# Optimization experiments

Measured on AMD Instinct MI355X. Metric: run time of the kernel, lower is better.

The kernel has to match this reference:

```python
import jax, jax.numpy as jnp
import numpy as np

B, N, D = 4096, 20, 256
MAX_STEPS = int(N * 1.5)  # exploration_ratio = 1.5


def setup_inputs() -> dict:
    key = jax.random.key(0)
    ks = jax.random.split(key, 9)
    s = 1.0 / np.sqrt(D)
    u = lambda k, shape: jax.random.uniform(k, shape, jnp.float32, -s, s)
    return {
        "node_emb": jax.random.normal(ks[0], (B, N, D), jnp.float32),
        "mask": jnp.ones((B, N), jnp.bool_),  # present in signature, unused by forward
        "W_ih": u(ks[1], (4 * D, D)),
        "W_hh": u(ks[2], (4 * D, D)),
        "b_ih": u(ks[3], (4 * D,)),
        "b_hh": u(ks[4], (4 * D,)),
        "attn_w": u(ks[5], (D, D)),
        "attn_b": u(ks[6], (D,)),
        "done_w": u(ks[7], (D,)),
        "done_b": u(ks[8], ()),
        "revisit_penalty": jnp.float32(-0.05),
        "greedy": 1,
    }


def reference(node_emb, mask, W_ih, W_hh, b_ih, b_hh, attn_w, attn_b, done_w, done_b, revisit_penalty, greedy):
    Bx, Nx, Dx = node_emb.shape
    aB = jnp.arange(Bx)
    aN = jnp.arange(Nx)
    scale = 1.0 / jnp.sqrt(jnp.float32(Dx))
    keys = node_emb @ attn_w.T + attn_b  # [B, N, D], loop-invariant

    def step(carry, t):
        h, c, inp, visited, unique, complete, first = carry
        # LSTMCell (PyTorch gate order i, f, g, o)
        gates = inp @ W_ih.T + b_ih + h @ W_hh.T + b_hh
        i, f, g, o = jnp.split(gates, 4, axis=1)
        c2 = jax.nn.sigmoid(f) * c + jax.nn.sigmoid(i) * jnp.tanh(g)
        h2 = jax.nn.sigmoid(o) * jnp.tanh(c2)
        # done predictor (greedy: complete when sigmoid > 0.5)
        done_p = jax.nn.sigmoid(h2 @ done_w + done_b)  # [B]
        eligible = (~complete) & (unique >= Nx) & (t >= Nx)
        complete2 = complete | (eligible & (done_p > 0.5))
        # pointer scores
        scores = jnp.einsum('bd,bnd->bn', h2, keys) * scale
        rev = ((~complete2) & (unique < Nx))[:, None] & visited
        scores = jnp.where(rev, revisit_penalty, scores)
        scores = jnp.where(complete2[:, None], jnp.float32(-1e9), scores)
        scores = jnp.where(complete2[:, None] & (aN[None, :] == first[:, None]), jnp.float32(100.0), scores)
        probs = jax.nn.softmax(scores, axis=1)
        choice = jnp.argmax(probs, axis=1).astype(jnp.int32)
        curr = jnp.where(complete2, first, choice)
        logp = jnp.log(probs[aB, curr] + 1e-10)
        first2 = jnp.where(t == 0, curr, first)
        newly = (~complete2) & (~visited[aB, curr])
        unique2 = unique + newly.astype(jnp.int32)
        visited2 = visited.at[aB, curr].set(visited[aB, curr] | (~complete2))
        inp2 = node_emb[aB, curr]
        return (h2, c2, inp2, visited2, unique2, complete2, first2), (curr, logp)

    init = (
        jnp.zeros((Bx, Dx), jnp.float32),
        jnp.zeros((Bx, Dx), jnp.float32),
        node_emb.mean(axis=1),
        jnp.zeros((Bx, Nx), jnp.bool_),
        jnp.zeros((Bx,), jnp.int32),
        jnp.zeros((Bx,), jnp.bool_),
        jnp.zeros((Bx,), jnp.int32),
    )
    carry, (tours_t, logps_t) = jax.lax.scan(step, init, jnp.arange(MAX_STEPS))
    complete, first = carry[5], carry[6]
    # step == max_steps: incomplete tours are closed at first_node, log-prob 0
    final_node = jnp.where(~complete, first, jnp.int32(0))
    tours = jnp.concatenate([tours_t.T, final_node[:, None]], axis=1)   # [B, MAX_STEPS+1]
    logps = jnp.concatenate([logps_t.T, jnp.zeros((Bx, 1), jnp.float32)], axis=1)
    return tours, logps
```

## Files before the change

### kernel.cpp

```cpp
#include <hip/hip_runtime.h>
#include <cstdint>
#include <cstddef>

#define NB   4096
#define NN   20
#define DD   256
#define TST  30
#define RPB  16
#define NTHR 512
#define SCALE 0.0625f

__device__ __forceinline__ float sigf(float x) {
    return 1.0f / (1.0f + expf(-x));
}

__global__ __launch_bounds__(256) void keys_gemm(
    const float* __restrict__ A, const float* __restrict__ W,
    const float* __restrict__ bias, float* __restrict__ C)
{
    __shared__ float As[64][33];
    __shared__ float Bs[64][33];
    const int bm = blockIdx.x * 64;
    const int bn = blockIdx.y * 64;
    const int t  = threadIdx.x;
    const int tm = t >> 4, tn = t & 15;
    const int sr = t >> 3;
    const int sk = (t & 7) << 2;
    float acc[4][4] = {};
    for (int k0 = 0; k0 < DD; k0 += 32) {
        __syncthreads();
#pragma unroll
        for (int p = 0; p < 2; ++p) {
            const int r = sr + p * 32;
            const float4 va = *(const float4*)&A[(size_t)(bm + r) * DD + k0 + sk];
            As[r][sk] = va.x; As[r][sk + 1] = va.y; As[r][sk + 2] = va.z; As[r][sk + 3] = va.w;
            const float4 vb = *(const float4*)&W[(size_t)(bn + r) * DD + k0 + sk];
            Bs[r][sk] = vb.x; Bs[r][sk + 1] = vb.y; Bs[r][sk + 2] = vb.z; Bs[r][sk + 3] = vb.w;
        }
        __syncthreads();
#pragma unroll
        for (int k = 0; k < 32; ++k) {
            float a[4], b[4];
#pragma unroll
            for (int i = 0; i < 4; ++i) a[i] = As[tm * 4 + i][k];
#pragma unroll
            for (int j = 0; j < 4; ++j) b[j] = Bs[tn * 4 + j][k];
#pragma unroll
            for (int i = 0; i < 4; ++i)
#pragma unroll
                for (int j = 0; j < 4; ++j)
                    acc[i][j] = fmaf(a[i], b[j], acc[i][j]);
        }
    }
#pragma unroll
    for (int i = 0; i < 4; ++i) {
        const int row = bm + tm * 4 + i;
#pragma unroll
        for (int j = 0; j < 4; ++j) {
            const int col = bn + tn * 4 + j;
            C[(size_t)row * DD + col] = acc[i][j] + bias[col];
        }
    }
}

__global__ __launch_bounds__(512) void decode(
    const float* __restrict__ ne,
    const float* __restrict__ wih,
    const float* __restrict__ whh,
    const float* __restrict__ bih,
    const float* __restrict__ bhh,
    const float* __restrict__ dwv,
    const float* __restrict__ dbp,
    const float* __restrict__ rpp,
    const float* __restrict__ keys,
    float* __restrict__ out)
{
    __shared__ float xcat[RPB][512];
    __shared__ float cst[RPB][DD];
    __shared__ float wt[512 * 32];
    __shared__ unsigned vis[RPB];
    __shared__ int uniq[RPB];
    __shared__ int firstn[RPB];
    __shared__ int compl_[RPB];

    const int t    = threadIdx.x;
    const int b0   = blockIdx.x * RPB;
    const int mg   = t >> 7;
    const int ni3  = t & 127;
    const int w    = t >> 6;
    const int lane = t & 63;

    const float done_b = dbp[0];
    const float rp     = rpp[0];

    float bsv[8];
#pragma unroll
    for (int g = 0; g < 8; ++g) {
        const int j = (g >> 1) * 256 + ((g & 1) << 7) + ni3;
        bsv[g] = bih[j] + bhh[j];
    }

    for (int idx = t; idx < RPB * DD; idx += NTHR) {
        const int r = idx >> 8, d = idx & 255;
        xcat[r][256 + d] = 0.0f;
        cst[r][d] = 0.0f;
    }
#pragma unroll
    for (int rr = 0; rr < 2; ++rr) {
        const int r = w * 2 + rr;
        const int b = b0 + r;
        float sx = 0.f, sy = 0.f, sz = 0.f, sw = 0.f;
        for (int n = 0; n < NN; ++n) {
            const float4 v = *(const float4*)&ne[((size_t)b * NN + n) * DD + lane * 4];
            sx += v.x; sy += v.y; sz += v.z; sw += v.w;
        }
        float4 m4;
        m4.x = sx / 20.0f; m4.y = sy / 20.0f; m4.z = sz / 20.0f; m4.w = sw / 20.0f;
        *(float4*)&xcat[r][lane * 4] = m4;
    }
    if (t < RPB) { vis[t] = 0u; uniq[t] = 0; firstn[t] = 0; compl_[t] = 0; }
    __syncthreads();

    auto stage = [&](int half, int k0) {
        __syncthreads();
        const float* base = (k0 < 256) ? (wih + k0) : (whh + (k0 - 256));
        const int rl = t >> 3;
        const int q4 = t & 7;
#pragma unroll
        for (int p = 0; p < 8; ++p) {
            const int row = rl + (p << 6);
            const float4 v = *(const float4*)&base[(size_t)(half * 512 + row) * DD + (q4 << 2)];
            *(float4*)&wt[(row << 5) + ((q4 ^ (row & 7)) << 2)] = v;
        }
        __syncthreads();
    };

    auto gemm_chunk = [&](int k0, float (&acc)[4][4]) {
#pragma unroll
        for (int q = 0; q < 8; ++q) {
            float4 av[4];
#pragma unroll
            for (int i = 0; i < 4; ++i)
                av[i] = *(const float4*)&xcat[(mg << 2) + i][k0 + (q << 2)];
            float4 wv[4];
#pragma unroll
            for (int c = 0; c < 4; ++c) {
                const int row = ni3 + (c << 7);
                wv[c] = *(const float4*)&wt[(row << 5) + ((q ^ (row & 7)) << 2)];
            }
#pragma unroll
            for (int i = 0; i < 4; ++i)
#pragma unroll
                for (int c = 0; c < 4; ++c) {
                    acc[i][c] = fmaf(av[i].x, wv[c].x, acc[i][c]);
                    acc[i][c] = fmaf(av[i].y, wv[c].y, acc[i][c]);
                    acc[i][c] = fmaf(av[i].z, wv[c].z, acc[i][c]);
                    acc[i][c] = fmaf(av[i].w, wv[c].w, acc[i][c]);
                }
        }
    };

    for (int step = 0; step < TST; ++step) {
        float acc0[4][4] = {};
        float acc1[4][4] = {};
#pragma unroll 1
        for (int kc = 0; kc < 16; ++kc) { stage(0, kc * 32); gemm_chunk(kc * 32, acc0); }
#pragma unroll 1
        for (int kc = 0; kc < 16; ++kc) { stage(1, kc * 32); gemm_chunk(kc * 32, acc1); }
        __syncthreads();

#pragma unroll
        for (int i = 0; i < 4; ++i) {
            const int r = (mg << 2) + i;
#pragma unroll
            for (int dd = 0; dd < 2; ++dd) {
                const int d = ni3 + (dd << 7);
                const float gi = acc0[i][dd]     + bsv[0 + dd];
                const float gf = acc0[i][2 + dd] + bsv[2 + dd];
                const float gg = acc1[i][dd]     + bsv[4 + dd];
                const float go = acc1[i][2 + dd] + bsv[6 + dd];
                const float co = cst[r][d];
                const float cn = sigf(gf) * co + sigf(gi) * tanhf(gg);
                const float hn = sigf(go) * tanhf(cn);
                cst[r][d] = cn;
                xcat[r][256 + d] = hn;
            }
        }
        __syncthreads();

#pragma unroll
        for (int rr = 0; rr < 2; ++rr) {
            const int r = w * 2 + rr;
            const int b = b0 + r;
            const float4 h4 = *(const float4*)&xcat[r][256 + lane * 4];

            const float4 dv = *(const float4*)&dwv[lane * 4];
            float pd = h4.x * dv.x + h4.y * dv.y + h4.z * dv.z + h4.w * dv.w;
#pragma unroll
            for (int o = 32; o >= 1; o >>= 1) pd += __shfl_xor(pd, o);

            float myscore = 0.0f;
            for (int n = 0; n < NN; ++n) {
                const float4 kv = *(const float4*)&keys[((size_t)b * NN + n) * DD + lane * 4];
                float sc = h4.x * kv.x + h4.y * kv.y + h4.z * kv.z + h4.w * kv.w;
#pragma unroll
                for (int o = 32; o >= 1; o >>= 1) sc += __shfl_xor(sc, o);
                if (lane == n) myscore = sc;
            }

            const unsigned vm0 = vis[r];
            int un = uniq[r];
            int fn = firstn[r];
            const int cm = compl_[r];

            const float dprob = 1.0f / (1.0f + expf(-(pd + done_b)));
            const int eligible = (!cm) && (un >= NN) && (step >= NN);
            const int cm2 = cm || (eligible && (dprob > 0.5f));

            float s;
            if (lane < NN) {
                s = myscore * SCALE;
                if ((!cm2) && (un < NN) && ((vm0 >> lane) & 1u)) s = rp;
                if (cm2) s = (lane == fn) ? 100.0f : -1e9f;
            } else {
                s = -INFINITY;
            }
            float m = s;
#pragma unroll
            for (int o = 32; o >= 1; o >>= 1) m = fmaxf(m, __shfl_xor(m, o));
            const float e = (lane < NN) ? expf(s - m) : 0.0f;
            float se = e;
#pragma unroll
            for (int o = 32; o >= 1; o >>= 1) se += __shfl_xor(se, o);
            const float p = e / se;
            float pm = p;
#pragma unroll
            for (int o = 32; o >= 1; o >>= 1) pm = fmaxf(pm, __shfl_xor(pm, o));
            const unsigned long long bal = __ballot(p == pm);
            const int choice = __ffsll(bal) - 1;
            const int curr = cm2 ? fn : choice;
            const float pc = __shfl(p, curr);
            const float lp = logf(pc + 1e-10f);

            if (step == 0) fn = curr;
            const int newly = (!cm2) && !((vm0 >> curr) & 1u);
            unsigned vm = vm0;
            if (!cm2) vm |= (1u << curr);
            un += newly;

            if (lane == 0) {
                vis[r] = vm; uniq[r] = un; firstn[r] = fn; compl_[r] = cm2;
                out[(size_t)b * (TST + 1) + step] = (float)curr;
                out[(size_t)NB * (TST + 1) + (size_t)b * (TST + 1) + step] = lp;
            }
            const float4 nv = *(const float4*)&ne[((size_t)b * NN + curr) * DD + lane * 4];
            *(float4*)&xcat[r][lane * 4] = nv;
        }
    }

    __syncthreads();
    if (t < RPB) {
        const int b = b0 + t;
        out[(size_t)b * (TST + 1) + TST] = compl_[t] ? 0.0f : (float)firstn[t];
        out[(size_t)NB * (TST + 1) + (size_t)b * (TST + 1) + TST] = 0.0f;
    }
}

extern "C" void kernel_launch(void* const* d_in, const int* in_sizes, int n_in,
                              void* d_out, int out_size, void* d_ws, size_t ws_size,
                              hipStream_t stream) {
    (void)in_sizes; (void)n_in; (void)out_size;
    const float* ne  = (const float*)d_in[0];
    const float* wih = (const float*)d_in[2];
    const float* whh = (const float*)d_in[3];
    const float* bih = (const float*)d_in[4];
    const float* bhh = (const float*)d_in[5];
    const float* aw  = (const float*)d_in[6];
    const float* ab  = (const float*)d_in[7];
    const float* dw  = (const float*)d_in[8];
    const float* db  = (const float*)d_in[9];
    const float* rp  = (const float*)d_in[10];
    float* out  = (float*)d_out;
    float* keys = (float*)d_ws;
    if (ws_size < (size_t)NB * NN * DD * sizeof(float)) return;

    keys_gemm<<<dim3((NB * NN) / 64, DD / 64), 256, 0, stream>>>(ne, aw, ab, keys);
    decode<<<dim3(NB / RPB), NTHR, 0, stream>>>(ne, wih, whh, bih, bhh, dw, db, rp, keys, out);
}
```

Baseline: 5.221 ms.

## Stream LSTM weights from global into registers with split-K halves, drop LDS staging

Replaces the per-chunk LDS staging of W_ih/W_hh, which cost two block barriers per chunk, with direct register loads that are double-buffered. Each thread computes 16 rows by 4 gate columns over one K half (input or hidden), and the two halves are reduced through a shared gates buffer. Cell state and the per-row tour state move into registers. The pointer softmax is now computed per lane over all 20 nodes, removing the shuffle reductions. This raises register pressure to about 64 accumulators plus 16 float4 weights, and requests 2 blocks per CU via launch bounds, which may cause spills.

```diff
diff --git a/kernel.cpp b/kernel.cpp
--- a/kernel.cpp
+++ b/kernel.cpp
@@ -63,7 +63,7 @@
     }
 }
 
-__global__ __launch_bounds__(512) void decode(
+__global__ __launch_bounds__(NTHR, 2) void decode(
     const float* __restrict__ ne,
     const float* __restrict__ wih,
     const float* __restrict__ whh,
@@ -76,19 +76,17 @@
     float* __restrict__ out)
 {
     __shared__ float xcat[RPB][512];
-    __shared__ float cst[RPB][DD];
-    __shared__ float wt[512 * 32];
-    __shared__ unsigned vis[RPB];
-    __shared__ int uniq[RPB];
-    __shared__ int firstn[RPB];
-    __shared__ int compl_[RPB];
+    __shared__ float gates[RPB][1024];
 
     const int t    = threadIdx.x;
     const int b0   = blockIdx.x * RPB;
+    const int lane = t & 63;
+    const int w    = t >> 6;
+    const int kh   = t >> 8;
+    const int q    = (t >> 6) & 3;
     const int mg   = t >> 7;
     const int ni3  = t & 127;
-    const int w    = t >> 6;
-    const int lane = t & 63;
+    const int xb   = kh << 8;
 
     const float done_b = dbp[0];
     const float rp     = rpp[0];
@@ -99,12 +97,16 @@
         const int j = (g >> 1) * 256 + ((g & 1) << 7) + ni3;
         bsv[g] = bih[j] + bhh[j];
     }
-
-    for (int idx = t; idx < RPB * DD; idx += NTHR) {
-        const int r = idx >> 8, d = idx & 255;
-        xcat[r][256 + d] = 0.0f;
-        cst[r][d] = 0.0f;
-    }
+    const float4 dv = *(const float4*)&dwv[lane * 4];
+
+    const float* Wb = kh ? whh : wih;
+    const float* p0 = Wb + (size_t)(q * 256 + 0 * 64 + lane) * DD;
+    const float* p1 = Wb + (size_t)(q * 256 + 1 * 64 + lane) * DD;
+    const float* p2 = Wb + (size_t)(q * 256 + 2 * 64 + lane) * DD;
+    const float* p3 = Wb + (size_t)(q * 256 + 3 * 64 + lane) * DD;
+
+    for (int idx = t; idx < RPB * 256; idx += NTHR)
+        xcat[idx >> 8][256 + (idx & 255)] = 0.0f;
 #pragma unroll
     for (int rr = 0; rr < 2; ++rr) {
         const int r = w * 2 + rr;
@@ -118,55 +120,75 @@
         m4.x = sx / 20.0f; m4.y = sy / 20.0f; m4.z = sz / 20.0f; m4.w = sw / 20.0f;
         *(float4*)&xcat[r][lane * 4] = m4;
     }
-    if (t < RPB) { vis[t] = 0u; uniq[t] = 0; firstn[t] = 0; compl_[t] = 0; }
-    __syncthreads();
-
-    auto stage = [&](int half, int k0) {
-        __syncthreads();
-        const float* base = (k0 < 256) ? (wih + k0) : (whh + (k0 - 256));
-        const int rl = t >> 3;
-        const int q4 = t & 7;
-#pragma unroll
-        for (int p = 0; p < 8; ++p) {
-            const int row = rl + (p << 6);
-            const float4 v = *(const float4*)&base[(size_t)(half * 512 + row) * DD + (q4 << 2)];
-            *(float4*)&wt[(row << 5) + ((q4 ^ (row & 7)) << 2)] = v;
-        }
-        __syncthreads();
+
+    float creg[4][2] = {};
+    unsigned vm[2] = {0u, 0u};
+    int un[2] = {0, 0}, fn[2] = {0, 0}, cm[2] = {0, 0};
+
+    auto ldw = [&](int k, float4 (&W)[4][2]) {
+#pragma unroll
+        for (int j = 0; j < 2; ++j) {
+            W[0][j] = *(const float4*)(p0 + k + j * 4);
+            W[1][j] = *(const float4*)(p1 + k + j * 4);
+            W[2][j] = *(const float4*)(p2 + k + j * 4);
+            W[3][j] = *(const float4*)(p3 + k + j * 4);
+        }
     };
 
-    auto gemm_chunk = [&](int k0, float (&acc)[4][4]) {
-#pragma unroll
-        for (int q = 0; q < 8; ++q) {
-            float4 av[4];
-#pragma unroll
-            for (int i = 0; i < 4; ++i)
-                av[i] = *(const float4*)&xcat[(mg << 2) + i][k0 + (q << 2)];
-            float4 wv[4];
-#pragma unroll
-            for (int c = 0; c < 4; ++c) {
-                const int row = ni3 + (c << 7);
-                wv[c] = *(const float4*)&wt[(row << 5) + ((q ^ (row & 7)) << 2)];
-            }
-#pragma unroll
-            for (int i = 0; i < 4; ++i)
-#pragma unroll
-                for (int c = 0; c < 4; ++c) {
-                    acc[i][c] = fmaf(av[i].x, wv[c].x, acc[i][c]);
-                    acc[i][c] = fmaf(av[i].y, wv[c].y, acc[i][c]);
-                    acc[i][c] = fmaf(av[i].z, wv[c].z, acc[i][c]);
-                    acc[i][c] = fmaf(av[i].w, wv[c].w, acc[i][c]);
+    for (int step = 0; step < TST; ++step) {
+        __syncthreads();
+
+        float acc[16][4] = {};
+        float4 wA[4][2], wB[4][2];
+        ldw(0, wA);
+#pragma unroll 1
+        for (int kc = 0; kc < 32; kc += 2) {
+            const int kA = kc * 8;
+            ldw(kA + 8, wB);
+#pragma unroll
+            for (int g = 0; g < 2; ++g)
+#pragma unroll
+                for (int r = 0; r < 16; ++r) {
+                    const float4 x4 = *(const float4*)&xcat[r][xb + kA + g * 4];
+#pragma unroll
+                    for (int c = 0; c < 4; ++c) {
+                        acc[r][c] = fmaf(x4.x, wA[c][g].x, acc[r][c]);
+                        acc[r][c] = fmaf(x4.y, wA[c][g].y, acc[r][c]);
+                        acc[r][c] = fmaf(x4.z, wA[c][g].z, acc[r][c]);
+                        acc[r][c] = fmaf(x4.w, wA[c][g].w, acc[r][c]);
+                    }
                 }
-        }
-    };
-
-    for (int step = 0; step < TST; ++step) {
-        float acc0[4][4] = {};
-        float acc1[4][4] = {};
-#pragma unroll 1
-        for (int kc = 0; kc < 16; ++kc) { stage(0, kc * 32); gemm_chunk(kc * 32, acc0); }
-#pragma unroll 1
-        for (int kc = 0; kc < 16; ++kc) { stage(1, kc * 32); gemm_chunk(kc * 32, acc1); }
+            if (kc + 2 < 32) ldw(kA + 16, wA);
+#pragma unroll
+            for (int g = 0; g < 2; ++g)
+#pragma unroll
+                for (int r = 0; r < 16; ++r) {
+                    const float4 x4 = *(const float4*)&xcat[r][xb + kA + 8 + g * 4];
+#pragma unroll
+                    for (int c = 0; c < 4; ++c) {
+                        acc[r][c] = fmaf(x4.x, wB[c][g].x, acc[r][c]);
+                        acc[r][c] = fmaf(x4.y, wB[c][g].y, acc[r][c]);
+                        acc[r][c] = fmaf(x4.z, wB[c][g].z, acc[r][c]);
+                        acc[r][c] = fmaf(x4.w, wB[c][g].w, acc[r][c]);
+                    }
+                }
+        }
+
+        if (kh == 0) {
+#pragma unroll
+            for (int r = 0; r < 16; ++r)
+#pragma unroll
+                for (int c = 0; c < 4; ++c)
+                    gates[r][q * 256 + c * 64 + lane] = acc[r][c];
+        }
+        __syncthreads();
+        if (kh == 1) {
+#pragma unroll
+            for (int r = 0; r < 16; ++r)
+#pragma unroll
+                for (int c = 0; c < 4; ++c)
+                    gates[r][q * 256 + c * 64 + lane] += acc[r][c];
+        }
         __syncthreads();
 
 #pragma unroll
@@ -175,14 +197,14 @@
 #pragma unroll
             for (int dd = 0; dd < 2; ++dd) {
                 const int d = ni3 + (dd << 7);
-                const float gi = acc0[i][dd]     + bsv[0 + dd];
-                const float gf = acc0[i][2 + dd] + bsv[2 + dd];
-                const float gg = acc1[i][dd]     + bsv[4 + dd];
-                const float go = acc1[i][2 + dd] + bsv[6 + dd];
-                const float co = cst[r][d];
+                const float gi = gates[r][d]       + bsv[0 + dd];
+                const float gf = gates[r][d + 256] + bsv[2 + dd];
+                const float gg = gates[r][d + 512] + bsv[4 + dd];
+                const float go = gates[r][d + 768] + bsv[6 + dd];
+                const float co = creg[i][dd];
                 const float cn = sigf(gf) * co + sigf(gi) * tanhf(gg);
                 const float hn = sigf(go) * tanhf(cn);
-                cst[r][d] = cn;
+                creg[i][dd] = cn;
                 xcat[r][256 + d] = hn;
             }
         }
@@ -194,62 +216,60 @@
             const int b = b0 + r;
             const float4 h4 = *(const float4*)&xcat[r][256 + lane * 4];
 
-            const float4 dv = *(const float4*)&dwv[lane * 4];
             float pd = h4.x * dv.x + h4.y * dv.y + h4.z * dv.z + h4.w * dv.w;
 #pragma unroll
             for (int o = 32; o >= 1; o >>= 1) pd += __shfl_xor(pd, o);
 
-            float myscore = 0.0f;
+            float ps[NN];
+            const float* kb = keys + (size_t)b * NN * DD + lane * 4;
+#pragma unroll
             for (int n = 0; n < NN; ++n) {
-                const float4 kv = *(const float4*)&keys[((size_t)b * NN + n) * DD + lane * 4];
-                float sc = h4.x * kv.x + h4.y * kv.y + h4.z * kv.z + h4.w * kv.w;
-#pragma unroll
-                for (int o = 32; o >= 1; o >>= 1) sc += __shfl_xor(sc, o);
-                if (lane == n) myscore = sc;
-            }
-
-            const unsigned vm0 = vis[r];
-            int un = uniq[r];
-            int fn = firstn[r];
-            const int cm = compl_[r];
+                const float4 kv = *(const float4*)(kb + n * DD);
+                ps[n] = h4.x * kv.x + h4.y * kv.y + h4.z * kv.z + h4.w * kv.w;
+            }
+#pragma unroll
+            for (int n = 0; n < NN; ++n) {
+                float v = ps[n];
+#pragma unroll
+                for (int o = 32; o >= 1; o >>= 1) v += __shfl_xor(v, o);
+                ps[n] = v;
+            }
 
             const float dprob = 1.0f / (1.0f + expf(-(pd + done_b)));
-            const int eligible = (!cm) && (un >= NN) && (step >= NN);
-            const int cm2 = cm || (eligible && (dprob > 0.5f));
-
-            float s;
-            if (lane < NN) {
-                s = myscore * SCALE;
-                if ((!cm2) && (un < NN) && ((vm0 >> lane) & 1u)) s = rp;
-                if (cm2) s = (lane == fn) ? 100.0f : -1e9f;
-            } else {
-                s = -INFINITY;
-            }
-            float m = s;
-#pragma unroll
-            for (int o = 32; o >= 1; o >>= 1) m = fmaxf(m, __shfl_xor(m, o));
-            const float e = (lane < NN) ? expf(s - m) : 0.0f;
-            float se = e;
-#pragma unroll
-            for (int o = 32; o >= 1; o >>= 1) se += __shfl_xor(se, o);
-            const float p = e / se;
-            float pm = p;
-#pragma unroll
-            for (int o = 32; o >= 1; o >>= 1) pm = fmaxf(pm, __shfl_xor(pm, o));
-            const unsigned long long bal = __ballot(p == pm);
-            const int choice = __ffsll(bal) - 1;
-            const int curr = cm2 ? fn : choice;
-            const float pc = __shfl(p, curr);
-            const float lp = logf(pc + 1e-10f);
-
-            if (step == 0) fn = curr;
-            const int newly = (!cm2) && !((vm0 >> curr) & 1u);
-            unsigned vm = vm0;
-            if (!cm2) vm |= (1u << curr);
-            un += newly;
+            const int elig = (!cm[rr]) && (un[rr] >= NN) && (step >= NN);
+            const int cm2  = cm[rr] || (elig && (dprob > 0.5f));
+
+            float sv[NN];
+#pragma unroll
+            for (int n = 0; n < NN; ++n) {
+                float s = ps[n] * SCALE;
+                if ((!cm2) && (un[rr] < NN) && ((vm[rr] >> n) & 1u)) s = rp;
+                if (cm2) s = (n == fn[rr]) ? 100.0f : -1e9f;
+                sv[n] = s;
+            }
+            float m = sv[0];
+#pragma unroll
+            for (int n = 1; n < NN; ++n) m = fmaxf(m, sv[n]);
+            float e[NN]; float se = 0.0f;
+#pragma unroll
+            for (int n = 0; n < NN; ++n) { e[n] = expf(sv[n] - m); se += e[n]; }
+            float pmax = e[0] / se; int idx = 0;
+#pragma unroll
+            for (int n = 1; n < NN; ++n) {
+                const float pn = e[n] / se;
+                if (pn > pmax) { pmax = pn; idx = n; }
+            }
+            const int curr  = cm2 ? fn[rr] : idx;
+            const float pc  = cm2 ? 1.0f : pmax;
+            const float lp  = logf(pc + 1e-10f);
+
+            if (step == 0) fn[rr] = curr;
+            const int newly = (!cm2) && !((vm[rr] >> curr) & 1u);
+            if (!cm2) vm[rr] |= (1u << curr);
+            un[rr] += newly;
+            cm[rr] = cm2;
 
             if (lane == 0) {
-                vis[r] = vm; uniq[r] = un; firstn[r] = fn; compl_[r] = cm2;
                 out[(size_t)b * (TST + 1) + step] = (float)curr;
                 out[(size_t)NB * (TST + 1) + (size_t)b * (TST + 1) + step] = lp;
             }
@@ -258,11 +278,13 @@
         }
     }
 
-    __syncthreads();
-    if (t < RPB) {
-        const int b = b0 + t;
-        out[(size_t)b * (TST + 1) + TST] = compl_[t] ? 0.0f : (float)firstn[t];
-        out[(size_t)NB * (TST + 1) + (size_t)b * (TST + 1) + TST] = 0.0f;
+#pragma unroll
+    for (int rr = 0; rr < 2; ++rr) {
+        const int b = b0 + w * 2 + rr;
+        if (lane == 0) {
+            out[(size_t)b * (TST + 1) + TST] = cm[rr] ? 0.0f : (float)fn[rr];
+            out[(size_t)NB * (TST + 1) + (size_t)b * (TST + 1) + TST] = 0.0f;
+        }
     }
 }
 
```

New measurement: 8.721 ms. +67.0%, slower.
